# Kernel tuning notes

Hardware: AMD Instinct MI355X
Metric: run time of the kernel (lower is better)

The kernel has to match this reference:

```python
import jax, jax.numpy as jnp
import numpy as np

COORD_DIM = 4
HIDDEN = 256
N_HIDDEN_LAYERS = 4  # num_layers - 1 hidden->hidden layers after the first
MIN_OMEGA = 10.0
MAX_OMEGA = 100.0
MEDIAN_OMEGA = (MIN_OMEGA + MAX_OMEGA) / 2.0
N = 524288


def _uniform(key, shape, bound):
    return jax.random.uniform(key, shape, jnp.float32, -bound, bound)


def setup_inputs() -> dict:
    key = jax.random.key(0)
    ks = jax.random.split(key, 16)
    coords = jax.random.normal(ks[0], (N, COORD_DIM), jnp.float32)
    # omega predictor: Linear(4, 64) -> ReLU -> Linear(64, 1) -> Sigmoid
    ow1 = _uniform(ks[1], (COORD_DIM, HIDDEN // 4), 1.0 / np.sqrt(COORD_DIM))
    ob1 = _uniform(ks[2], (HIDDEN // 4,), 1.0 / np.sqrt(COORD_DIM))
    ow2 = _uniform(ks[3], (HIDDEN // 4, 1), 1.0 / np.sqrt(HIDDEN // 4))
    ob2 = _uniform(ks[4], (1,), 1.0 / np.sqrt(HIDDEN // 4))
    # SIREN first layer: uniform(-1/in_features, 1/in_features)
    w0 = _uniform(ks[5], (COORD_DIM, HIDDEN), 1.0 / COORD_DIM)
    b0 = _uniform(ks[6], (HIDDEN,), 1.0 / np.sqrt(COORD_DIM))
    # SIREN hidden layers: uniform(-sqrt(6/in)/omega0, ...), stacked [4, 256, 256]
    hb = np.sqrt(6.0 / HIDDEN) / MEDIAN_OMEGA
    wh = _uniform(ks[7], (N_HIDDEN_LAYERS, HIDDEN, HIDDEN), hb)
    bh = _uniform(ks[8], (N_HIDDEN_LAYERS, HIDDEN), 1.0 / np.sqrt(HIDDEN))
    wf = _uniform(ks[9], (HIDDEN, 1), hb)
    bf = _uniform(ks[10], (1,), 1.0 / np.sqrt(HIDDEN))
    return {"coords": coords, "ow1": ow1, "ob1": ob1, "ow2": ow2, "ob2": ob2,
            "w0": w0, "b0": b0, "wh": wh, "bh": bh, "wf": wf, "bf": bf}


def reference(coords, ow1, ob1, ow2, ob2, w0, b0, wh, bh, wf, bf):
    # adaptive omega per coordinate: [N, 1]
    h = jax.nn.relu(coords @ ow1 + ob1)
    omega = MIN_OMEGA + (MAX_OMEGA - MIN_OMEGA) * jax.nn.sigmoid(h @ ow2 + ob2)
    # SIREN stack: x = sin(omega * (x @ W + b))
    x = jnp.sin(omega * (coords @ w0 + b0))
    for i in range(N_HIDDEN_LAYERS):
        x = jnp.sin(omega * (x @ wh[i] + bh[i]))
    return x @ wf + bf  # [N, 1]
```

## Files before the change

### kernel.cpp

```cpp
#include <hip/hip_runtime.h>
#include <hip/hip_bf16.h>

typedef _Float16 f16;
typedef f16 f16x4 __attribute__((ext_vector_type(4)));
typedef f16 f16x8 __attribute__((ext_vector_type(8)));
typedef __fp16 h16x2 __attribute__((ext_vector_type(2)));
typedef __fp16 h16x4 __attribute__((ext_vector_type(4)));
typedef float f32x4 __attribute__((ext_vector_type(4)));
typedef float f32x16 __attribute__((ext_vector_type(16)));

#define MT 64
#define LDST 260
#define INV2PI 0.15915494309189535f

__global__ __launch_bounds__(64)
void prep_wt(const float* __restrict__ wh, f16* __restrict__ wt) {
    const int b = blockIdx.x;
    const int layer = b >> 7, wcblk = (b >> 4) & 7, kblk = b & 15;
    const int lane = threadIdx.x;
    const int l31 = lane & 31, lh = lane >> 5;
    const float* src = wh + layer * 65536 + (kblk * 16 + lh * 8) * 256 + wcblk * 32 + l31;
    f16x8 v;
#pragma unroll
    for (int j = 0; j < 8; j++) v[j] = (f16)src[j * 256];
    *(f16x8*)(wt + b * 512 + lane * 8) = v;
}

__device__ inline f16x8 lds_ld8(const f16* p) {
    f16x4 lo = *(const f16x4*)p;
    f16x4 hi = *(const f16x4*)(p + 4);
    return __builtin_shufflevector(lo, hi, 0, 1, 2, 3, 4, 5, 6, 7);
}

__device__ inline f16x4 pk4(float z0, float z1, float z2, float z3) {
    h16x2 a = __builtin_amdgcn_cvt_pkrtz(z0, z1);
    h16x2 b = __builtin_amdgcn_cvt_pkrtz(z2, z3);
    h16x4 r = __builtin_shufflevector(a, b, 0, 1, 2, 3);
    return __builtin_bit_cast(f16x4, r);
}

__global__ __launch_bounds__(256, 2)
void siren_fused(const float* __restrict__ coords,
                 const float* __restrict__ ow1, const float* __restrict__ ob1,
                 const float* __restrict__ ow2, const float* __restrict__ ob2,
                 const float* __restrict__ w0, const float* __restrict__ b0,
                 const f16* __restrict__ wt,
                 const float* __restrict__ bh,
                 const float* __restrict__ wf,
                 const float* __restrict__ bf,
                 float* __restrict__ out) {
    __shared__ __align__(16) f16 Xs[2][MT * LDST];
    __shared__ float om_rev[MT];
    __shared__ __align__(16) float crd[MT * 4];
    __shared__ __align__(16) float wf_s[256];

    const int t = threadIdx.x;
    const long base_pt = (long)blockIdx.x * MT;

    if (t < MT) ((f32x4*)crd)[t] = ((const f32x4*)(coords + base_pt * 4))[t];
    wf_s[t] = wf[t];
    __syncthreads();

    if (t < MT) {
        const float c0 = crd[t * 4], c1 = crd[t * 4 + 1], c2 = crd[t * 4 + 2], c3 = crd[t * 4 + 3];
        float h[64];
#pragma unroll
        for (int j = 0; j < 64; j++) {
            float z = ob1[j] + c0 * ow1[j] + c1 * ow1[64 + j] + c2 * ow1[128 + j] + c3 * ow1[192 + j];
            h[j] = fmaxf(z, 0.f);
        }
        float z2 = ob2[0];
#pragma unroll
        for (int j = 0; j < 64; j++) z2 += h[j] * ow2[j];
        const float sig = 1.f / (1.f + __expf(-z2));
        om_rev[t] = (10.f + 90.f * sig) * INV2PI;
    }
    __syncthreads();

    {
        const int pt = t >> 2;
        const int q = t & 3;
        const float c0 = crd[pt * 4], c1 = crd[pt * 4 + 1], c2 = crd[pt * 4 + 2], c3 = crd[pt * 4 + 3];
        const float orv = om_rev[pt];
#pragma unroll
        for (int i = 0; i < 4; i++) {
            const int ch = (q + 4 * i) * 16;
#pragma unroll
            for (int c = 0; c < 16; c += 4) {
                f32x4 wv0 = *(const f32x4*)(w0 + 0 * 256 + ch + c);
                f32x4 wv1 = *(const f32x4*)(w0 + 1 * 256 + ch + c);
                f32x4 wv2 = *(const f32x4*)(w0 + 2 * 256 + ch + c);
                f32x4 wv3 = *(const f32x4*)(w0 + 3 * 256 + ch + c);
                f32x4 bv  = *(const f32x4*)(b0 + ch + c);
                float z[4];
#pragma unroll
                for (int j = 0; j < 4; j++) {
                    float zz = bv[j] + c0 * wv0[j] + c1 * wv1[j] + c2 * wv2[j] + c3 * wv3[j];
                    z[j] = __builtin_amdgcn_sinf(orv * zz);
                }
                *(f16x4*)&Xs[0][pt * LDST + ch + c] = pk4(z[0], z[1], z[2], z[3]);
            }
        }
    }
    __syncthreads();

    const int lane = t & 63;
    const int wave = t >> 6;
    const int l31 = lane & 31;
    const int lh = lane >> 5;
    const int wc0 = wave * 64;

    for (int layer = 0; layer < 4; layer++) {
        const int cur = layer & 1;

        const f16* afrag = wt + ((layer * 8 + wave * 2) * 16) * 512 + lane * 8;
        const f16* bptr = &Xs[cur][l31 * LDST + lh * 8];

        f32x16 acc[2][2];
#pragma unroll
        for (int ct = 0; ct < 2; ct++)
#pragma unroll
            for (int g = 0; g < 4; g++) {
                f32x4 bb = *(const f32x4*)(bh + layer * 256 + wc0 + ct * 32 + g * 8 + lh * 4);
#pragma unroll
                for (int j = 0; j < 4; j++) {
                    acc[ct][0][g * 4 + j] = bb[j];
                    acc[ct][1][g * 4 + j] = bb[j];
                }
            }

        f16x8 a0[3], a1[3];
#pragma unroll
        for (int d = 0; d < 3; d++) {
            a0[d] = *(const f16x8*)(afrag + d * 512);
            a1[d] = *(const f16x8*)(afrag + 8192 + d * 512);
        }
        f16x8 bv0 = lds_ld8(bptr);
        f16x8 bv1 = lds_ld8(bptr + 32 * LDST);

#pragma unroll
        for (int kb = 0; kb < 16; kb++) {
            const int s = kb % 3;
            f16x8 av0 = a0[s], av1 = a1[s];
            if (kb + 3 < 16) {
                a0[s] = *(const f16x8*)(afrag + (kb + 3) * 512);
                a1[s] = *(const f16x8*)(afrag + 8192 + (kb + 3) * 512);
            }
            f16x8 b0v = bv0, b1v = bv1;
            if (kb + 1 < 16) {
                bv0 = lds_ld8(bptr + (kb + 1) * 16);
                bv1 = lds_ld8(bptr + 32 * LDST + (kb + 1) * 16);
            }
            acc[0][0] = __builtin_amdgcn_mfma_f32_32x32x16_f16(av0, b0v, acc[0][0], 0, 0, 0);
            acc[0][1] = __builtin_amdgcn_mfma_f32_32x32x16_f16(av0, b1v, acc[0][1], 0, 0, 0);
            acc[1][0] = __builtin_amdgcn_mfma_f32_32x32x16_f16(av1, b0v, acc[1][0], 0, 0, 0);
            acc[1][1] = __builtin_amdgcn_mfma_f32_32x32x16_f16(av1, b1v, acc[1][1], 0, 0, 0);
        }

        float orv[2];
        orv[0] = om_rev[l31];
        orv[1] = om_rev[32 + l31];
#pragma unroll
        for (int ct = 0; ct < 2; ct++) {
#pragma unroll
            for (int g = 0; g < 4; g++) {
                const int wc = wc0 + ct * 32 + g * 8 + lh * 4;
#pragma unroll
                for (int rt = 0; rt < 2; rt++) {
                    const int prow = rt * 32 + l31;
                    float z[4];
#pragma unroll
                    for (int j = 0; j < 4; j++)
                        z[j] = __builtin_amdgcn_sinf(orv[rt] * acc[ct][rt][g * 4 + j]);
                    *(f16x4*)&Xs[cur ^ 1][prow * LDST + wc] = pk4(z[0], z[1], z[2], z[3]);
                }
            }
        }
        __syncthreads();
    }

    {
        const int pt = t >> 2;
        const int q = t & 3;
        const f16* xrow = &Xs[0][pt * LDST];
        float s = 0.f;
#pragma unroll
        for (int i = 0; i < 4; i++) {
            const int ch = (q + 4 * i) * 16;
#pragma unroll
            for (int c = 0; c < 16; c += 4) {
                f16x4 xv = *(const f16x4*)(xrow + ch + c);
                f32x4 wv = *(const f32x4*)&wf_s[ch + c];
                s += (float)xv[0] * wv[0] + (float)xv[1] * wv[1]
                   + (float)xv[2] * wv[2] + (float)xv[3] * wv[3];
            }
        }
        s += __shfl_xor(s, 1, 64);
        s += __shfl_xor(s, 2, 64);
        if (q == 0) out[base_pt + pt] = s + bf[0];
    }
}

extern "C" void kernel_launch(void* const* d_in, const int* in_sizes, int n_in,
                              void* d_out, int out_size, void* d_ws, size_t ws_size,
                              hipStream_t stream) {
    (void)in_sizes; (void)n_in; (void)out_size; (void)ws_size;
    const float* coords = (const float*)d_in[0];
    const float* ow1 = (const float*)d_in[1];
    const float* ob1 = (const float*)d_in[2];
    const float* ow2 = (const float*)d_in[3];
    const float* ob2 = (const float*)d_in[4];
    const float* w0  = (const float*)d_in[5];
    const float* b0  = (const float*)d_in[6];
    const float* wh  = (const float*)d_in[7];
    const float* bh  = (const float*)d_in[8];
    const float* wf  = (const float*)d_in[9];
    const float* bf  = (const float*)d_in[10];
    float* out = (float*)d_out;
    f16* wt = (f16*)d_ws;

    prep_wt<<<512, 64, 0, stream>>>(wh, wt);
    siren_fused<<<524288 / MT, 256, 0, stream>>>(coords, ow1, ob1, ow2, ob2,
                                                 w0, b0, wt, bh, wf, bf, out);
}
```

Before: 506.3 us.

## Single-buffer activation tile in LDS and raise occupancy to four blocks per CU

The double-buffered activation tile in shared memory becomes a single buffer, with an extra barrier between the MFMA reads and the sine write-back. This halves LDS use per block (about 66KB to 33KB), and launch bounds are raised to request four resident blocks per CU. The B-operand software prefetch is dropped and the layer loop is kept rolled. In exchange the extra barrier per layer and the tighter register budget may cause stalls or spills.

```diff
diff --git a/kernel.cpp b/kernel.cpp
--- a/kernel.cpp
+++ b/kernel.cpp
@@ -39,7 +39,7 @@
     return __builtin_bit_cast(f16x4, r);
 }
 
-__global__ __launch_bounds__(256, 2)
+__global__ __launch_bounds__(256, 4)
 void siren_fused(const float* __restrict__ coords,
                  const float* __restrict__ ow1, const float* __restrict__ ob1,
                  const float* __restrict__ ow2, const float* __restrict__ ob2,
@@ -49,7 +49,7 @@
                  const float* __restrict__ wf,
                  const float* __restrict__ bf,
                  float* __restrict__ out) {
-    __shared__ __align__(16) f16 Xs[2][MT * LDST];
+    __shared__ __align__(16) f16 Xs[MT * LDST];
     __shared__ float om_rev[MT];
     __shared__ __align__(16) float crd[MT * 4];
     __shared__ __align__(16) float wf_s[256];
@@ -98,7 +98,7 @@
                     float zz = bv[j] + c0 * wv0[j] + c1 * wv1[j] + c2 * wv2[j] + c3 * wv3[j];
                     z[j] = __builtin_amdgcn_sinf(orv * zz);
                 }
-                *(f16x4*)&Xs[0][pt * LDST + ch + c] = pk4(z[0], z[1], z[2], z[3]);
+                *(f16x4*)&Xs[pt * LDST + ch + c] = pk4(z[0], z[1], z[2], z[3]);
             }
         }
     }
@@ -110,11 +110,10 @@
     const int lh = lane >> 5;
     const int wc0 = wave * 64;
 
+#pragma unroll 1
     for (int layer = 0; layer < 4; layer++) {
-        const int cur = layer & 1;
-
         const f16* afrag = wt + ((layer * 8 + wave * 2) * 16) * 512 + lane * 8;
-        const f16* bptr = &Xs[cur][l31 * LDST + lh * 8];
+        const f16* bptr = &Xs[l31 * LDST + lh * 8];
 
         f32x16 acc[2][2];
 #pragma unroll
@@ -135,8 +134,6 @@
             a0[d] = *(const f16x8*)(afrag + d * 512);
             a1[d] = *(const f16x8*)(afrag + 8192 + d * 512);
         }
-        f16x8 bv0 = lds_ld8(bptr);
-        f16x8 bv1 = lds_ld8(bptr + 32 * LDST);
 
 #pragma unroll
         for (int kb = 0; kb < 16; kb++) {
@@ -146,16 +143,14 @@
                 a0[s] = *(const f16x8*)(afrag + (kb + 3) * 512);
                 a1[s] = *(const f16x8*)(afrag + 8192 + (kb + 3) * 512);
             }
-            f16x8 b0v = bv0, b1v = bv1;
-            if (kb + 1 < 16) {
-                bv0 = lds_ld8(bptr + (kb + 1) * 16);
-                bv1 = lds_ld8(bptr + 32 * LDST + (kb + 1) * 16);
-            }
-            acc[0][0] = __builtin_amdgcn_mfma_f32_32x32x16_f16(av0, b0v, acc[0][0], 0, 0, 0);
-            acc[0][1] = __builtin_amdgcn_mfma_f32_32x32x16_f16(av0, b1v, acc[0][1], 0, 0, 0);
-            acc[1][0] = __builtin_amdgcn_mfma_f32_32x32x16_f16(av1, b0v, acc[1][0], 0, 0, 0);
-            acc[1][1] = __builtin_amdgcn_mfma_f32_32x32x16_f16(av1, b1v, acc[1][1], 0, 0, 0);
-        }
+            f16x8 bv0 = lds_ld8(bptr + 0 * 32 * LDST + kb * 16);
+            f16x8 bv1 = lds_ld8(bptr + 1 * 32 * LDST + kb * 16);
+            acc[0][0] = __builtin_amdgcn_mfma_f32_32x32x16_f16(av0, bv0, acc[0][0], 0, 0, 0);
+            acc[0][1] = __builtin_amdgcn_mfma_f32_32x32x16_f16(av0, bv1, acc[0][1], 0, 0, 0);
+            acc[1][0] = __builtin_amdgcn_mfma_f32_32x32x16_f16(av1, bv0, acc[1][0], 0, 0, 0);
+            acc[1][1] = __builtin_amdgcn_mfma_f32_32x32x16_f16(av1, bv1, acc[1][1], 0, 0, 0);
+        }
+        __syncthreads();
 
         float orv[2];
         orv[0] = om_rev[l31];
@@ -172,7 +167,7 @@
 #pragma unroll
                     for (int j = 0; j < 4; j++)
                         z[j] = __builtin_amdgcn_sinf(orv[rt] * acc[ct][rt][g * 4 + j]);
-                    *(f16x4*)&Xs[cur ^ 1][prow * LDST + wc] = pk4(z[0], z[1], z[2], z[3]);
+                    *(f16x4*)&Xs[prow * LDST + wc] = pk4(z[0], z[1], z[2], z[3]);
                 }
             }
         }
@@ -182,7 +177,7 @@
     {
         const int pt = t >> 2;
         const int q = t & 3;
-        const f16* xrow = &Xs[0][pt * LDST];
+        const f16* xrow = &Xs[pt * LDST];
         float s = 0.f;
 #pragma unroll
         for (int i = 0; i < 4; i++) {
```

Measured after the change: 447.0 us. -11.7%, faster.
